# Kernel tuning notes

Measured on AMD Instinct MI355X. Metric: run time of the kernel, lower is better.

## Reference

```python
import jax, jax.numpy as jnp
import numpy as np

B, H, N, P = 2, 8, 2048, 64   # batch, heads, seq, head_dim
M, D = 4, 256                 # sketch count, sketch feature dim


def setup_inputs() -> dict:
    key = jax.random.key(0)
    kq, kk, ks, kr = jax.random.split(key, 4)
    scale = P ** -0.5  # keep exp(QK) numerically tame, std(dot) ~= 1/8
    Q = jax.random.normal(kq, (B, H, N, P), dtype=jnp.float32) * scale
    K = jax.random.normal(kk, (B, H, N, P), dtype=jnp.float32) * scale
    # indices into the concatenated [Q;K] token axis of length 2N
    sketching_matrix = jax.random.randint(ks, (B, M, D), 0, 2 * N)
    # Rademacher random signs, broadcast over [b,h,2n] in the reduction
    random_sign = jnp.sign(jax.random.normal(kr, (M, D), dtype=jnp.float32))
    random_sign = jnp.where(random_sign == 0, 1.0, random_sign)
    return {"Q": Q, "K": K, "sketching_matrix": sketching_matrix,
            "random_sign": random_sign}


def reference(Q, K, sketching_matrix, random_sign):
    b, h, n, p = Q.shape
    X = jnp.concatenate([Q, K], axis=2)          # [b,h,2n,p]
    Xt = jnp.transpose(X, (0, 2, 1, 3))          # [b,2n,h,p]
    # gather sketched landmarks: [b,m,d,h,p] -> [b,h,m,d,p]
    XS = Xt[jnp.arange(b)[:, None, None], sketching_matrix]
    XS = jnp.transpose(XS, (0, 3, 1, 2, 4))
    # RS_SM accumulate branch: exp of inner products, random-sign reduce over m
    product = jnp.einsum('bhnp,bhmdp->bhnmd', X, XS)   # [b,h,2n,m,d]
    AS = jnp.einsum('bhnmd,md->bhnd', jnp.exp(product), random_sign)
    return AS.astype(Q.dtype)                    # [b,h,2n,d]
```

## Files before the change

### kernel.cpp

```cpp
#include <hip/hip_runtime.h>
#include <hip/hip_bf16.h>

typedef __attribute__((ext_vector_type(8))) short short8;
typedef __attribute__((ext_vector_type(4))) float f32x4;

namespace {
constexpr int Nc  = 2048;
constexpr int NXc = 4096;
constexpr int Pc  = 64;
constexpr int Mc  = 4;
constexpr int Dc  = 256;
constexpr int BH  = 16;
constexpr float LOG2E = 1.4426950408889634f;
}

__device__ inline float fexp2(float x) {
#if __has_builtin(__builtin_amdgcn_exp2f)
  return __builtin_amdgcn_exp2f(x);
#else
  return exp2f(x);
#endif
}

__device__ inline unsigned int bfpack(float a, float b) {
  union { __hip_bfloat162 h; unsigned int u; } cv;
  cv.h = __float22bfloat162_rn(make_float2(a, b));
  return cv.u;
}

__global__ __launch_bounds__(256, 4) void sketch_fused(
    const float* __restrict__ Q, const float* __restrict__ K,
    const int* __restrict__ SK, const float* __restrict__ SGN,
    float* __restrict__ OUT)
{
  __shared__ __hip_bfloat16 Ws[Mc * 64 * Pc];

  const int t    = threadIdx.x;
  const int lane = t & 63;
  const int wv   = t >> 6;
  const int brow = lane & 15;
  const int q    = lane >> 4;
  const int bh   = blockIdx.y;
  const int b    = bh >> 3;

  const int bx  = blockIdx.x;
  const int xcd = bx & 7;
  const int rr  = bx >> 3;
  const int nch = xcd * 2 + (rr >> 2);
  const int dq  = rr & 3;
  const int n0  = nch * 256;
  const int d0  = dq * 64;

  char* wsb = (char*)Ws;

  {
    const int dl = t >> 2;
    const int qt = t & 3;
    const int* skp = SK + b * (Mc * Dc) + d0 + dl;
    const int sw = (dl & 7) << 4;
    #pragma unroll
    for (int m = 0; m < 4; ++m) {
      const int idx = skp[m * Dc];
      const float* src = ((idx < Nc) ? (Q + ((size_t)bh * Nc + idx) * Pc)
                                     : (K + ((size_t)bh * Nc + (idx - Nc)) * Pc))
                         + qt * 16;
      f32x4 f0 = *(const f32x4*)(src);
      f32x4 f1 = *(const f32x4*)(src + 4);
      f32x4 f2 = *(const f32x4*)(src + 8);
      f32x4 f3 = *(const f32x4*)(src + 12);
      uint4 ua, ub;
      ua.x = bfpack(f0.x * LOG2E, f0.y * LOG2E);
      ua.y = bfpack(f0.z * LOG2E, f0.w * LOG2E);
      ua.z = bfpack(f1.x * LOG2E, f1.y * LOG2E);
      ua.w = bfpack(f1.z * LOG2E, f1.w * LOG2E);
      ub.x = bfpack(f2.x * LOG2E, f2.y * LOG2E);
      ub.y = bfpack(f2.z * LOG2E, f2.w * LOG2E);
      ub.z = bfpack(f3.x * LOG2E, f3.y * LOG2E);
      ub.w = bfpack(f3.z * LOG2E, f3.w * LOG2E);
      char* rp = wsb + (m * 64 + dl) * 128;
      *(uint4*)(rp + ((qt * 32) ^ sw))      = ua;
      *(uint4*)(rp + ((qt * 32 + 16) ^ sw)) = ub;
    }
  }
  __syncthreads();

  const float* xr = ((n0 < Nc) ? (Q + ((size_t)bh * Nc + n0) * Pc)
                               : (K + ((size_t)bh * Nc + (n0 - Nc)) * Pc))
                    + (size_t)(wv * 64 + brow) * Pc + q * 8;
  short8 b0[4], b1[4];
  #pragma unroll
  for (int tt = 0; tt < 4; ++tt) {
    const float* xp = xr + (size_t)tt * 16 * Pc;
    f32x4 x0 = *(const f32x4*)(xp);
    f32x4 x1 = *(const f32x4*)(xp + 4);
    f32x4 x2 = *(const f32x4*)(xp + 32);
    f32x4 x3 = *(const f32x4*)(xp + 36);
    union { short8 s; uint4 u; } c0, c1;
    c0.u.x = bfpack(x0.x, x0.y); c0.u.y = bfpack(x0.z, x0.w);
    c0.u.z = bfpack(x1.x, x1.y); c0.u.w = bfpack(x1.z, x1.w);
    c1.u.x = bfpack(x2.x, x2.y); c1.u.y = bfpack(x2.z, x2.w);
    c1.u.z = bfpack(x3.x, x3.y); c1.u.w = bfpack(x3.z, x3.w);
    b0[tt] = c0.s; b1[tt] = c1.s;
  }

  const int swr = (brow & 7) << 4;
  float* obase = OUT + ((size_t)bh * NXc + n0 + wv * 64 + brow) * Dc + d0 + q * 4;

  #pragma unroll
  for (int dt = 0; dt < 4; ++dt) {
    f32x4 acc[4];
    #pragma unroll
    for (int tt = 0; tt < 4; ++tt) acc[tt] = (f32x4){0.f, 0.f, 0.f, 0.f};

    #pragma unroll
    for (int m = 0; m < 4; ++m) {
      const char* ap = wsb + (m * 64 + dt * 16 + brow) * 128;
      short8 a0 = *(const short8*)(ap + ((q * 16) ^ swr));
      short8 a1 = *(const short8*)(ap + ((64 + q * 16) ^ swr));
      const f32x4 sg = *(const f32x4*)(SGN + m * Dc + d0 + dt * 16 + q * 4);
      #pragma unroll
      for (int tt = 0; tt < 4; ++tt) {
        f32x4 c = {0.f, 0.f, 0.f, 0.f};
        c = __builtin_amdgcn_mfma_f32_16x16x32_bf16(a0, b0[tt], c, 0, 0, 0);
        c = __builtin_amdgcn_mfma_f32_16x16x32_bf16(a1, b1[tt], c, 0, 0, 0);
        acc[tt].x = fmaf(sg.x, fexp2(c.x), acc[tt].x);
        acc[tt].y = fmaf(sg.y, fexp2(c.y), acc[tt].y);
        acc[tt].z = fmaf(sg.z, fexp2(c.z), acc[tt].z);
        acc[tt].w = fmaf(sg.w, fexp2(c.w), acc[tt].w);
      }
    }

    #pragma unroll
    for (int tt = 0; tt < 4; ++tt) {
      *(f32x4*)(obase + (size_t)tt * 16 * Dc + dt * 16) = acc[tt];
    }
  }
}

extern "C" void kernel_launch(void* const* d_in, const int* in_sizes, int n_in,
                              void* d_out, int out_size, void* d_ws, size_t ws_size,
                              hipStream_t stream) {
  (void)in_sizes; (void)n_in; (void)out_size; (void)d_ws; (void)ws_size;
  const float* Q   = (const float*)d_in[0];
  const float* K   = (const float*)d_in[1];
  const int*   SK  = (const int*)d_in[2];
  const float* SGN = (const float*)d_in[3];
  float* OUT = (float*)d_out;

  sketch_fused<<<dim3(64, BH), dim3(256), 0, stream>>>(Q, K, SK, SGN, OUT);
}
```

Measured before the change: 104.5 us.

## Split landmark gather into bf16 prepass kernel, hoist X loads, nontemporal output stores

Moves the indexed gather, LOG2E scaling and bf16 conversion of sketched landmarks into a separate prepass kernel that writes a compact bf16 buffer to workspace. The main kernel then streams contiguous bf16 rows into LDS instead of doing four redundant scattered fp32 gathers per block. It also issues the token-row global loads before the barrier so they overlap the LDS fill, and writes the output with nontemporal stores. The cost is an extra kernel launch and a workspace round trip.

New measurement: 106.5 us. No clear change (+1.9%).

```diff
diff --git a/kernel.cpp b/kernel.cpp
--- a/kernel.cpp
+++ b/kernel.cpp
@@ -28,10 +28,33 @@
   return cv.u;
 }
 
-__global__ __launch_bounds__(256, 4) void sketch_fused(
+__global__ __launch_bounds__(256) void prepass_kernel(
     const float* __restrict__ Q, const float* __restrict__ K,
-    const int* __restrict__ SK, const float* __restrict__ SGN,
-    float* __restrict__ OUT)
+    const int* __restrict__ SK, __hip_bfloat16* __restrict__ Wb)
+{
+  const int t  = blockIdx.x * 256 + threadIdx.x;
+  const int q  = t & 7;
+  const int r  = t >> 3;
+  const int bh = r >> 10;
+  const int md = r & 1023;
+  const int b  = bh >> 3;
+  const int idx = SK[b * (Mc * Dc) + md];
+  const float* src = (idx < Nc) ? (Q + ((size_t)bh * Nc + idx) * Pc)
+                                : (K + ((size_t)bh * Nc + (idx - Nc)) * Pc);
+  const f32x4* s4 = (const f32x4*)(src + q * 8);
+  f32x4 f0 = s4[0], f1 = s4[1];
+  uint4 u;
+  u.x = bfpack(f0.x * LOG2E, f0.y * LOG2E);
+  u.y = bfpack(f0.z * LOG2E, f0.w * LOG2E);
+  u.z = bfpack(f1.x * LOG2E, f1.y * LOG2E);
+  u.w = bfpack(f1.z * LOG2E, f1.w * LOG2E);
+  *(uint4*)(Wb + (size_t)r * Pc + q * 8) = u;
+}
+
+__global__ __launch_bounds__(256, 4) void sketch_main(
+    const float* __restrict__ Q, const float* __restrict__ K,
+    const __hip_bfloat16* __restrict__ Wb,
+    const float* __restrict__ SGN, float* __restrict__ OUT)
 {
   __shared__ __hip_bfloat16 Ws[Mc * 64 * Pc];
 
@@ -41,7 +64,6 @@
   const int brow = lane & 15;
   const int q    = lane >> 4;
   const int bh   = blockIdx.y;
-  const int b    = bh >> 3;
 
   const int bx  = blockIdx.x;
   const int xcd = bx & 7;
@@ -56,46 +78,40 @@
   {
     const int dl = t >> 2;
     const int qt = t & 3;
-    const int* skp = SK + b * (Mc * Dc) + d0 + dl;
     const int sw = (dl & 7) << 4;
+    const __hip_bfloat16* wsrc =
+        Wb + ((size_t)bh * (Mc * Dc) + d0 + dl) * Pc + qt * 16;
     #pragma unroll
     for (int m = 0; m < 4; ++m) {
-      const int idx = skp[m * Dc];
-      const float* src = ((idx < Nc) ? (Q + ((size_t)bh * Nc + idx) * Pc)
-                                     : (K + ((size_t)bh * Nc + (idx - Nc)) * Pc))
-                         + qt * 16;
-      f32x4 f0 = *(const f32x4*)(src);
-      f32x4 f1 = *(const f32x4*)(src + 4);
-      f32x4 f2 = *(const f32x4*)(src + 8);
-      f32x4 f3 = *(const f32x4*)(src + 12);
-      uint4 ua, ub;
-      ua.x = bfpack(f0.x * LOG2E, f0.y * LOG2E);
-      ua.y = bfpack(f0.z * LOG2E, f0.w * LOG2E);
-      ua.z = bfpack(f1.x * LOG2E, f1.y * LOG2E);
-      ua.w = bfpack(f1.z * LOG2E, f1.w * LOG2E);
-      ub.x = bfpack(f2.x * LOG2E, f2.y * LOG2E);
-      ub.y = bfpack(f2.z * LOG2E, f2.w * LOG2E);
-      ub.z = bfpack(f3.x * LOG2E, f3.y * LOG2E);
-      ub.w = bfpack(f3.z * LOG2E, f3.w * LOG2E);
+      uint4 wa = *(const uint4*)(wsrc + (size_t)m * Dc * Pc);
+      uint4 wb = *(const uint4*)(wsrc + (size_t)m * Dc * Pc + 8);
       char* rp = wsb + (m * 64 + dl) * 128;
-      *(uint4*)(rp + ((qt * 32) ^ sw))      = ua;
-      *(uint4*)(rp + ((qt * 32 + 16) ^ sw)) = ub;
+      *(uint4*)(rp + ((qt * 32) ^ sw))      = wa;
+      *(uint4*)(rp + ((qt * 32 + 16) ^ sw)) = wb;
     }
   }
-  __syncthreads();
 
   const float* xr = ((n0 < Nc) ? (Q + ((size_t)bh * Nc + n0) * Pc)
                                : (K + ((size_t)bh * Nc + (n0 - Nc)) * Pc))
                     + (size_t)(wv * 64 + brow) * Pc + q * 8;
+  f32x4 xv[16];
+  #pragma unroll
+  for (int tt = 0; tt < 4; ++tt) {
+    const float* xp = xr + (size_t)tt * 16 * Pc;
+    xv[tt * 4 + 0] = *(const f32x4*)(xp);
+    xv[tt * 4 + 1] = *(const f32x4*)(xp + 4);
+    xv[tt * 4 + 2] = *(const f32x4*)(xp + 32);
+    xv[tt * 4 + 3] = *(const f32x4*)(xp + 36);
+  }
+
+  __syncthreads();
+
   short8 b0[4], b1[4];
   #pragma unroll
   for (int tt = 0; tt < 4; ++tt) {
-    const float* xp = xr + (size_t)tt * 16 * Pc;
-    f32x4 x0 = *(const f32x4*)(xp);
-    f32x4 x1 = *(const f32x4*)(xp + 4);
-    f32x4 x2 = *(const f32x4*)(xp + 32);
-    f32x4 x3 = *(const f32x4*)(xp + 36);
     union { short8 s; uint4 u; } c0, c1;
+    f32x4 x0 = xv[tt * 4 + 0], x1 = xv[tt * 4 + 1];
+    f32x4 x2 = xv[tt * 4 + 2], x3 = xv[tt * 4 + 3];
     c0.u.x = bfpack(x0.x, x0.y); c0.u.y = bfpack(x0.z, x0.w);
     c0.u.z = bfpack(x1.x, x1.y); c0.u.w = bfpack(x1.z, x1.w);
     c1.u.x = bfpack(x2.x, x2.y); c1.u.y = bfpack(x2.z, x2.w);
@@ -132,7 +148,8 @@
 
     #pragma unroll
     for (int tt = 0; tt < 4; ++tt) {
-      *(f32x4*)(obase + (size_t)tt * 16 * Dc + dt * 16) = acc[tt];
+      __builtin_nontemporal_store(
+          acc[tt], (f32x4*)(obase + (size_t)tt * 16 * Dc + dt * 16));
     }
   }
 }
@@ -140,12 +157,15 @@
 extern "C" void kernel_launch(void* const* d_in, const int* in_sizes, int n_in,
                               void* d_out, int out_size, void* d_ws, size_t ws_size,
                               hipStream_t stream) {
-  (void)in_sizes; (void)n_in; (void)out_size; (void)d_ws; (void)ws_size;
+  (void)in_sizes; (void)n_in; (void)out_size; (void)ws_size;
   const float* Q   = (const float*)d_in[0];
   const float* K   = (const float*)d_in[1];
   const int*   SK  = (const int*)d_in[2];
   const float* SGN = (const float*)d_in[3];
   float* OUT = (float*)d_out;
 
-  sketch_fused<<<dim3(64, BH), dim3(256), 0, stream>>>(Q, K, SK, SGN, OUT);
+  __hip_bfloat16* Wb = (__hip_bfloat16*)d_ws;
+
+  prepass_kernel<<<dim3(512), dim3(256), 0, stream>>>(Q, K, SK, Wb);
+  sketch_main<<<dim3(64, BH), dim3(256), 0, stream>>>(Q, K, Wb, SGN, OUT);
 }
```
